# Kernel optimization log

Measured on AMD Instinct MI355X. Metric: run time of the kernel, lower is better.

The kernel has to match this reference:

```python
import jax, jax.numpy as jnp
import numpy as np

B, T_SRC, T_TGT = 2048, 32, 32
D = 512            # d_model
D_SRC, D_TGT = 100, 80
L = 2              # n_layers


def setup_inputs() -> dict:
    key = jax.random.key(0)
    ks = jax.random.split(key, 16)
    s = 1.0 / float(np.sqrt(D))  # torch LSTM init scale
    u = lambda k, shape: jax.random.uniform(k, shape, jnp.float32, -s, s)
    return {
        "src": jax.random.randint(ks[0], (B, T_SRC), 0, D_SRC, dtype=jnp.int32),
        "tgt": jax.random.randint(ks[1], (B, T_TGT), 0, D_TGT, dtype=jnp.int32),
        "enc_emb": jax.random.normal(ks[2], (D_SRC, D), jnp.float32),
        "dec_emb": jax.random.normal(ks[3], (D_TGT, D), jnp.float32),
        "enc_Wih": u(ks[4], (L, 4 * D, D)),
        "enc_Whh": u(ks[5], (L, 4 * D, D)),
        "enc_bih": u(ks[6], (L, 4 * D)),
        "enc_bhh": u(ks[7], (L, 4 * D)),
        "dec_Wih": u(ks[8], (L, 4 * D, D)),
        "dec_Whh": u(ks[9], (L, 4 * D, D)),
        "dec_bih": u(ks[10], (L, 4 * D)),
        "dec_bhh": u(ks[11], (L, 4 * D)),
        "post_W": u(ks[12], (D_TGT, D)),
        "post_b": u(ks[13], (D_TGT,)),
    }


def lstm_cell(x, h, c, Wih, Whh, bih, bhh):
    # PyTorch gate order: i, f, g, o
    gates = x @ Wih.T + bih + h @ Whh.T + bhh  # [B, 4D]
    i, f, g, o = jnp.split(gates, 4, axis=-1)
    c_new = jax.nn.sigmoid(f) * c + jax.nn.sigmoid(i) * jnp.tanh(g)
    h_new = jax.nn.sigmoid(o) * jnp.tanh(c_new)
    return h_new, c_new


def reference(src, tgt, enc_emb, dec_emb, enc_Wih, enc_Whh, enc_bih, enc_bhh,
              dec_Wih, dec_Whh, dec_bih, dec_bhh, post_W, post_b):
    # Eval-mode forward: dropout = identity, teacher forcing disabled
    # (tf = random() < ratio AND self.training is False at inference).
    n_layers = enc_Wih.shape[0]
    Bb = src.shape[0]
    Dm = enc_emb.shape[1]

    # ---- encoder: multi-layer LSTM over src embeddings ----
    x = enc_emb[src].swapaxes(0, 1)  # [T_src, B, D]
    hs, cs = [], []
    z = jnp.zeros((Bb, Dm), x.dtype)
    for l in range(n_layers):
        def step(carry, xt, l=l):
            h, c = carry
            h, c = lstm_cell(xt, h, c, enc_Wih[l], enc_Whh[l], enc_bih[l], enc_bhh[l])
            return (h, c), h
        (hT, cT), x = jax.lax.scan(step, (z, z), x)
        hs.append(hT)
        cs.append(cT)
    h0 = jnp.stack(hs)  # [L, B, D]
    c0 = jnp.stack(cs)  # [L, B, D]

    prev0 = dec_emb[tgt[:, 0]]  # [B, D]

    def dec_step(carry, _):
        h, c, prev = carry
        x = prev
        new_h, new_c = [], []
        for l in range(n_layers):
            hl, cl = lstm_cell(x, h[l], c[l], dec_Wih[l], dec_Whh[l], dec_bih[l], dec_bhh[l])
            new_h.append(hl)
            new_c.append(cl)
            x = hl
        logits = x @ post_W.T + post_b          # [B, d_tgt]
        pred = jnp.argmax(logits, axis=-1)       # [B]
        prev = dec_emb[pred]                     # [B, D]
        return (jnp.stack(new_h), jnp.stack(new_c), prev), logits

    _, out = jax.lax.scan(dec_step, (h0, c0, prev0), None, length=tgt.shape[1])
    return out.swapaxes(0, 1)  # [B, T_tgt, d_tgt]
```

## Files before the change

### kernel.cpp

```cpp
#include <hip/hip_runtime.h>
#include <hip/hip_bf16.h>

#define B_  2048
#define T_  32
#define D_  512
#define G_  2048
#define VT_ 80
#define BD  (B_ * D_)
#define LWE ((size_t)G_ * D_)

typedef _Float16 half8 __attribute__((ext_vector_type(8)));
typedef _Float16 half4_t __attribute__((ext_vector_type(4)));
typedef float    f32x4 __attribute__((ext_vector_type(4)));

static __device__ __forceinline__ float sigm(float x) {
    return 1.0f / (1.0f + expf(-x));
}

typedef __attribute__((address_space(1))) unsigned int gas_u32;
typedef __attribute__((address_space(3))) unsigned int las_u32;
static __device__ __forceinline__ void glds16(const void* src, void* dst) {
    __builtin_amdgcn_global_load_lds(
        (gas_u32*)(unsigned long long)(size_t)src,
        (las_u32*)(unsigned int)(size_t)dst, 16, 0, 0);
}

#define WB() do {                                         \
    asm volatile("s_waitcnt vmcnt(2)" ::: "memory");      \
    __builtin_amdgcn_s_barrier();                         \
    __builtin_amdgcn_sched_barrier(0);                    \
} while (0)

__global__ void zero_ws(int4* __restrict__ p, int n) {
    int i = blockIdx.x * blockDim.x + threadIdx.x;
    if (i < n) p[i] = int4{0, 0, 0, 0};
}
__global__ void init_pred(const int* __restrict__ tgt, int* __restrict__ pred) {
    int i = blockIdx.x * blockDim.x + threadIdx.x;
    if (i < B_) pred[i] = tgt[i * T_];
}

__global__ void split_weights(const float* __restrict__ s0, const float* __restrict__ s1,
                              const float* __restrict__ s2, const float* __restrict__ s3,
                              const float* __restrict__ s4, const float* __restrict__ s5,
                              _Float16* __restrict__ Wbase) {
    int g = blockIdx.x * blockDim.x + threadIdx.x;
    int mat = g >> 17;
    int rem = g & 131071;
    int np  = rem >> 6;
    int kq  = rem & 63;
    const float* src = (mat == 0) ? s0 : (mat == 1) ? s1 : (mat == 2) ? s2
                     : (mat == 3) ? s3 : (mat == 4) ? s4 : s5;
    int n = (np & 3) * D_ + (np >> 2);
    const float* sp = src + (size_t)n * D_ + kq * 8;
    float4 v0 = ((const float4*)sp)[0], v1 = ((const float4*)sp)[1];
    float x[8] = {v0.x, v0.y, v0.z, v0.w, v1.x, v1.y, v1.z, v1.w};
    _Float16 hi[8], lo[8];
    #pragma unroll
    for (int u = 0; u < 8; ++u) {
        hi[u] = (_Float16)x[u];
        lo[u] = (_Float16)(x[u] - (float)hi[u]);
    }
    int tile = (np >> 4) * 16 + (kq >> 2);
    int lane = (np & 15) | ((kq & 3) << 4);
    size_t e = (size_t)tile * 512 + (size_t)lane * 8;
    _Float16* Whi = Wbase + (size_t)mat * (2 * LWE);
    _Float16* Wlo = Whi + LWE;
    *(half8*)(Whi + e) = *(half8*)hi;
    *(half8*)(Wlo + e) = *(half8*)lo;
}

__global__ void split_postW(const float* __restrict__ pw,
                            _Float16* __restrict__ Ph, _Float16* __restrict__ Pl) {
    int g = blockIdx.x * blockDim.x + threadIdx.x;
    if (g >= VT_ * 64) return;
    int v = g >> 6, kq = g & 63;
    const float* sp = pw + (size_t)v * D_ + kq * 8;
    float4 v0 = ((const float4*)sp)[0], v1 = ((const float4*)sp)[1];
    float x[8] = {v0.x, v0.y, v0.z, v0.w, v1.x, v1.y, v1.z, v1.w};
    _Float16 hi[8], lo[8];
    #pragma unroll
    for (int u = 0; u < 8; ++u) {
        hi[u] = (_Float16)x[u];
        lo[u] = (_Float16)(x[u] - (float)hi[u]);
    }
    int tile = (v >> 4) * 16 + (kq >> 2);
    int lane = (v & 15) | ((kq & 3) << 4);
    size_t e = (size_t)tile * 512 + (size_t)lane * 8;
    *(half8*)(Ph + e) = *(half8*)hi;
    *(half8*)(Pl + e) = *(half8*)lo;
}

__global__ void perm_bias(const float* __restrict__ ebih, const float* __restrict__ ebhh,
                          const float* __restrict__ dbih, const float* __restrict__ dbhh,
                          float* __restrict__ biasP) {
    int i = blockIdx.x * blockDim.x + threadIdx.x;
    int cfg = i >> 11, np = i & 2047;
    int n = (np & 3) * D_ + (np >> 2);
    const float* bi = ((cfg < 2) ? ebih : dbih) + (cfg & 1) * G_;
    const float* bh = ((cfg < 2) ? ebhh : dbhh) + (cfg & 1) * G_;
    biasP[cfg * G_ + np] = bi[n] + bh[n];
}

__global__ __launch_bounds__(256) void compute_P(
    const float* __restrict__ enc_emb, const float* __restrict__ dec_emb,
    const float* __restrict__ encW0,   const float* __restrict__ decW0,
    float* __restrict__ P) {
    __shared__ float es[10][D_];
    __shared__ float part[4][64][10];
    int by = blockIdx.y;
    bool enc = (by < 10);
    int r0 = enc ? by * 10 : 100 + (by - 10) * 10;
    int s0 = enc ? by * 10 : (by - 10) * 10;
    const float* emb = enc ? enc_emb : dec_emb;
    const float* W   = enc ? encW0 : decW0;
    int tid = threadIdx.x;
    #pragma unroll
    for (int it = 0; it < 5; ++it) {
        int i4 = it * 256 + tid;
        int rr = i4 >> 7, cc = i4 & 127;
        ((float4*)es[rr])[cc] = ((const float4*)(emb + (size_t)(s0 + rr) * D_))[cc];
    }
    __syncthreads();
    int o   = tid & 63;
    int seg = tid >> 6;
    int np = blockIdx.x * 64 + o;
    int n = (np & 3) * D_ + (np >> 2);
    const float* wr = W + (size_t)n * D_ + seg * 128;
    float acc[10];
    #pragma unroll
    for (int rr = 0; rr < 10; ++rr) acc[rr] = 0.f;
    for (int k = 0; k < 128; k += 4) {
        float4 w4 = *(const float4*)(wr + k);
        int kb = seg * 128 + k;
        #pragma unroll
        for (int rr = 0; rr < 10; ++rr)
            acc[rr] += es[rr][kb] * w4.x + es[rr][kb+1] * w4.y
                     + es[rr][kb+2] * w4.z + es[rr][kb+3] * w4.w;
    }
    #pragma unroll
    for (int rr = 0; rr < 10; ++rr) part[seg][o][rr] = acc[rr];
    __syncthreads();
    for (int i = tid; i < 640; i += 256) {
        int o2 = i & 63, rr = i >> 6;
        P[(size_t)(r0 + rr) * G_ + blockIdx.x * 64 + o2] =
            (part[0][o2][rr] + part[1][o2][rr]) + (part[2][o2][rr] + part[3][o2][rr]);
    }
}

struct CellJob {
    const _Float16 *a0h, *a0l, *w0h, *w0l;
    int kclo0, kchi0;
    const _Float16 *a1h, *a1l, *w1h, *w1l;
    int kclo1, kchi1;
    const float *biasP;
    const float *P;
    const int  *idx;
    int idx_stride, emb_rows;
    float *c_io;
    _Float16 *hh_out, *hl_out;
};

__global__ __launch_bounds__(512, 2) void lstm_cell_mfma(CellJob J0, CellJob J1) {
    const CellJob J = (blockIdx.z == 0) ? J0 : J1;
    __shared__ __align__(128) char smem[65536];
    float (*gf)[68] = (float (*)[68])smem;

    const int tid  = threadIdx.x;
    const int w    = tid >> 6;
    const int lane = tid & 63;
    const int g    = w >> 2;
    const int mw   = w & 3;
    const int id   = blockIdx.x;
    const int bx   = id >> 3;
    const int m0   = (id & 7) * 256;

    const _Float16* Ah = g ? J.a1h : J.a0h;
    const _Float16* Al = g ? J.a1l : J.a0l;
    const _Float16* Wh = g ? J.w1h : J.w0h;
    const _Float16* Wl = g ? J.w1l : J.w0l;
    const int kclo = g ? J.kclo1 : J.kclo0;
    const int kchi = g ? J.kchi1 : J.kchi0;

    const int afr = (m0 >> 4) + mw * 4;
    const int wfr = bx * 4;

    f32x4 acc[4][4];
    #pragma unroll
    for (int i = 0; i < 4; ++i)
        #pragma unroll
        for (int j = 0; j < 4; ++j) acc[i][j] = f32x4{0.f, 0.f, 0.f, 0.f};

    char* const sb = smem + w * 2048;
    const char* const rg0 = smem + (g << 13);

    auto stage = [&](int buf, int kc) {
        size_t toff = (((size_t)(wfr + (w & 3)) * 16 + kc) << 9) + (size_t)lane * 8;
        char* d = sb + buf * 16384;
        glds16(Wh + toff, d);
        glds16(Wl + toff, d + 1024);
    };
    auto ldA = [&](half8* A8, int kc) {
        size_t lo8 = (size_t)lane * 8;
        #pragma unroll
        for (int i = 0; i < 4; ++i) {
            size_t off = (((size_t)(afr + i) * 16 + kc) << 9) + lo8;
            A8[i]     = *(const half8*)(Ah + off);
            A8[4 + i] = *(const half8*)(Al + off);
        }
    };
    auto domfma = [&](const half8* A8, int buf) {
        const char* r = rg0 + buf * 16384;
        size_t lo16 = (size_t)lane * 16;
        #pragma unroll
        for (int j = 0; j < 4; ++j) {
            half8 Bh = *(const half8*)(r + j * 2048 + lo16);
            half8 Bl = *(const half8*)(r + j * 2048 + 1024 + lo16);
            #pragma unroll
            for (int i = 0; i < 4; ++i) {
                acc[i][j] = __builtin_amdgcn_mfma_f32_16x16x32_f16(A8[i], Bh, acc[i][j], 0, 0, 0);
                acc[i][j] = __builtin_amdgcn_mfma_f32_16x16x32_f16(A8[i], Bl, acc[i][j], 0, 0, 0);
                acc[i][j] = __builtin_amdgcn_mfma_f32_16x16x32_f16(A8[4 + i], Bh, acc[i][j], 0, 0, 0);
            }
        }
    };

    half8 A0[8], A1[8];
    const int nit = (kchi - kclo) >> 2;

    ldA(A0, kclo);
    __builtin_amdgcn_sched_barrier(0);
    stage(0, kclo);
    stage(1, kclo + 1);
    WB();

    for (int it = 0; it < nit; ++it) {
        const int k0 = kclo + (it << 2);
        const bool more = (it + 1 < nit);

        ldA(A1, k0 + 1); __builtin_amdgcn_sched_barrier(0);
        stage(2, k0 + 2);
        domfma(A0, 0);
        WB();

        ldA(A0, k0 + 2); __builtin_amdgcn_sched_barrier(0);
        stage(3, k0 + 3);
        domfma(A1, 1);
        WB();

        ldA(A1, k0 + 3); __builtin_amdgcn_sched_barrier(0);
        if (more) stage(0, k0 + 4);
        domfma(A0, 2);
        WB();

        if (more) {
            ldA(A0, k0 + 4); __builtin_amdgcn_sched_barrier(0);
            stage(1, k0 + 5);
        }
        domfma(A1, 3);
        WB();
    }

    const int rbase = (lane >> 4) << 2;
    const int cbase = lane & 15;
    for (int p = 0; p < 2; ++p) {
        if (g == 0 && (mw >> 1) == p) {
            #pragma unroll
            for (int i = 0; i < 4; ++i) {
                int mrow = (mw & 1) * 64 + i * 16 + rbase;
                #pragma unroll
                for (int j = 0; j < 4; ++j) {
                    int nc = j * 16 + cbase;
                    #pragma unroll
                    for (int r = 0; r < 4; ++r)
                        gf[mrow + r][nc] = acc[i][j][r];
                }
            }
        }
        __syncthreads();
        if (g == 1 && (mw >> 1) == p) {
            #pragma unroll
            for (int i = 0; i < 4; ++i) {
                int mrow = (mw & 1) * 64 + i * 16 + rbase;
                #pragma unroll
                for (int j = 0; j < 4; ++j) {
                    int nc = j * 16 + cbase;
                    #pragma unroll
                    for (int r = 0; r < 4; ++r)
                        gf[mrow + r][nc] += acc[i][j][r];
                }
            }
        }
        __syncthreads();
        {
            int mr = tid >> 2, q = tid & 3;
            int mg = m0 + p * 128 + mr;
            const float4* brow = (const float4*)(J.biasP + (bx << 6));
            const float4* Pr = nullptr;
            if (J.P) {
                int s = J.idx[mg * J.idx_stride];
                s = min(max(s, 0), J.emb_rows - 1);
                Pr = (const float4*)(J.P + (size_t)s * G_ + (bx << 6));
            }
            float* crow = J.c_io + (size_t)mg * D_ + (bx << 4) + (q << 2);
            float4 cv = *(float4*)crow;
            _Float16 hh4[4], hl4[4];
            #pragma unroll
            for (int e = 0; e < 4; ++e) {
                int dl = (q << 2) + e;
                float4 g4 = *(float4*)&gf[mr][dl << 2];
                float4 b4 = brow[dl];
                float gi = g4.x + b4.x, gF = g4.y + b4.y;
                float gg = g4.z + b4.z, go = g4.w + b4.w;
                if (Pr) {
                    float4 p4 = Pr[dl];
                    gi += p4.x; gF += p4.y; gg += p4.z; go += p4.w;
                }
                float cc = (&cv.x)[e];
                float cn = sigm(gF) * cc + sigm(gi) * tanhf(gg);
                float hn = sigm(go) * tanhf(cn);
                (&cv.x)[e] = cn;
                _Float16 hH = (_Float16)hn;
                hh4[e] = hH;
                hl4[e] = (_Float16)(hn - (float)hH);
            }
            *(float4*)crow = cv;
            int kk = (bx << 4) + (q << 2);
            size_t hoff = ((size_t)((mg >> 4) * 16 + (kk >> 5)) << 9)
                        + (size_t)((mg & 15) | (((kk >> 3) & 3) << 4)) * 8
                        + ((q & 1) << 2);
            *(half4_t*)(J.hh_out + hoff) = *(half4_t*)hh4;
            *(half4_t*)(J.hl_out + hoff) = *(half4_t*)hl4;
        }
        __syncthreads();
    }
}

__global__ __launch_bounds__(128) void logits_mfma(
    const _Float16* __restrict__ Ah, const _Float16* __restrict__ Al,
    const _Float16* __restrict__ Bh, const _Float16* __restrict__ Bl,
    const float* __restrict__ postb, float* __restrict__ out,
    int t, int* __restrict__ pred) {
    __shared__ float gf2[64][85];
    __shared__ float pb[VT_];
    const int tid = threadIdx.x;
    const int w = tid >> 6;
    const int lane = tid & 63;
    const int m0 = blockIdx.x * 64;
    const int afr = blockIdx.x * 4;

    f32x4 acc[4][5];
    #pragma unroll
    for (int i = 0; i < 4; ++i)
        #pragma unroll
        for (int j = 0; j < 5; ++j) acc[i][j] = f32x4{0.f, 0.f, 0.f, 0.f};

    size_t lo8 = (size_t)lane * 8;
    for (int kc = w * 8; kc < w * 8 + 8; ++kc) {
        half8 A8[8], Bh8[5], Bl8[5];
        #pragma unroll
        for (int i = 0; i < 4; ++i) {
            size_t off = (((size_t)(afr + i) * 16 + kc) << 9) + lo8;
            A8[i]     = *(const half8*)(Ah + off);
            A8[4 + i] = *(const half8*)(Al + off);
        }
        #pragma unroll
        for (int j = 0; j < 5; ++j) {
            size_t off = (((size_t)(j * 16 + kc)) << 9) + lo8;
            Bh8[j] = *(const half8*)(Bh + off);
            Bl8[j] = *(const half8*)(Bl + off);
        }
        #pragma unroll
        for (int i = 0; i < 4; ++i)
            #pragma unroll
            for (int j = 0; j < 5; ++j) {
                acc[i][j] = __builtin_amdgcn_mfma_f32_16x16x32_f16(A8[i], Bh8[j], acc[i][j], 0, 0, 0);
                acc[i][j] = __builtin_amdgcn_mfma_f32_16x16x32_f16(A8[i], Bl8[j], acc[i][j], 0, 0, 0);
                acc[i][j] = __builtin_amdgcn_mfma_f32_16x16x32_f16(A8[4 + i], Bh8[j], acc[i][j], 0, 0, 0);
            }
    }

    if (tid < VT_) pb[tid] = postb[tid];
    const int quad = lane >> 4, c = lane & 15;
    if (w == 0) {
        #pragma unroll
        for (int i = 0; i < 4; ++i)
            #pragma unroll
            for (int j = 0; j < 5; ++j)
                #pragma unroll
                for (int r = 0; r < 4; ++r)
                    gf2[i * 16 + quad * 4 + r][j * 16 + c] = acc[i][j][r];
    }
    __syncthreads();
    if (w == 1) {
        #pragma unroll
        for (int i = 0; i < 4; ++i)
            #pragma unroll
            for (int j = 0; j < 5; ++j)
                #pragma unroll
                for (int r = 0; r < 4; ++r)
                    gf2[i * 16 + quad * 4 + r][j * 16 + c] += acc[i][j][r];
    }
    __syncthreads();
    if (tid < 64) {
        int r = tid;
        float best = -3.4e38f; int bi = 0;
        #pragma unroll
        for (int v = 0; v < VT_; ++v) {
            float x = gf2[r][v] + pb[v];
            if (x > best) { best = x; bi = v; }
        }
        pred[m0 + r] = bi;
        float* orow = out + (size_t)(m0 + r) * (T_ * VT_) + (size_t)t * VT_;
        #pragma unroll
        for (int v4 = 0; v4 < VT_ / 4; ++v4) {
            float4 g4 = *(float4*)&gf2[r][v4 * 4];
            float4 b4 = *(float4*)&pb[v4 * 4];
            float4 o4 = {g4.x + b4.x, g4.y + b4.y, g4.z + b4.z, g4.w + b4.w};
            *(float4*)(orow + v4 * 4) = o4;
        }
    }
}

extern "C" void kernel_launch(void* const* d_in, const int* in_sizes, int n_in,
                              void* d_out, int out_size, void* d_ws, size_t ws_size,
                              hipStream_t stream) {
    (void)in_sizes; (void)n_in; (void)out_size; (void)ws_size;

    const int*   src     = (const int*)d_in[0];
    const int*   tgt     = (const int*)d_in[1];
    const float* enc_emb = (const float*)d_in[2];
    const float* dec_emb = (const float*)d_in[3];
    const float* enc_Wih = (const float*)d_in[4];
    const float* enc_Whh = (const float*)d_in[5];
    const float* enc_bih = (const float*)d_in[6];
    const float* enc_bhh = (const float*)d_in[7];
    const float* dec_Wih = (const float*)d_in[8];
    const float* dec_Whh = (const float*)d_in[9];
    const float* dec_bih = (const float*)d_in[10];
    const float* dec_bhh = (const float*)d_in[11];
    const float* post_W  = (const float*)d_in[12];
    const float* post_b  = (const float*)d_in[13];

    char* wsb = (char*)d_ws;
    int*   pred  = (int*)wsb;
    float* biasB = (float*)(wsb + 16384);
    float* Ptab  = (float*)(wsb + 16384 + 32768);
    char*  zbase = wsb + 16384 + 32768 + 180 * G_ * 4;
    float* C0 = (float*)zbase;
    float* C1 = C0 + BD;
    _Float16* Hh00 = (_Float16*)(C1 + BD);
    _Float16* Hh10 = Hh00 + BD;
    _Float16* Hl00 = Hh10 + BD;
    _Float16* Hl10 = Hl00 + BD;
    _Float16* Hh01 = Hl10 + BD;
    _Float16* Hh11 = Hh01 + BD;
    _Float16* Hl01 = Hh11 + BD;
    _Float16* Hl11 = Hl01 + BD;
    _Float16* Wb   = Hl11 + BD;
    _Float16* PwH  = Wb + 6 * 2 * LWE;
    _Float16* PwL  = PwH + (size_t)VT_ * D_;

    _Float16* Hhi[2][2] = { { Hh00, Hh01 }, { Hh10, Hh11 } };
    _Float16* Hlo[2][2] = { { Hl00, Hl01 }, { Hl10, Hl11 } };
    float*    Cp[2]     = { C0, C1 };
    auto WP = [&](int m, int pl) { return Wb + (size_t)m * (2 * LWE) + (size_t)pl * LWE; };

    float* out = (float*)d_out;

    zero_ws<<<4096, 256, 0, stream>>>((int4*)zbase, (16 * 1024 * 1024) / 16);
    init_pred<<<8, 256, 0, stream>>>(tgt, pred);
    split_weights<<<3072, 256, 0, stream>>>(
        enc_Whh, enc_Wih + LWE, enc_Whh + LWE,
        dec_Whh, dec_Wih + LWE, dec_Whh + LWE, Wb);
    split_postW<<<20, 256, 0, stream>>>(post_W, PwH, PwL);
    perm_bias<<<32, 256, 0, stream>>>(enc_bih, enc_bhh, dec_bih, dec_bhh, biasB);
    {
        dim3 gP(32, 18);
        compute_P<<<gP, 256, 0, stream>>>(enc_emb, dec_emb, enc_Wih, dec_Wih, Ptab);
    }

    dim3 grid1(256, 1, 1);
    dim3 grid2(256, 1, 2);
    int c0 = 0, c1 = 0;

    auto mkL0 = [&](bool enc, const int* ix, int stride, int rows) {
        int m = enc ? 0 : 3;
        CellJob j;
        j.a0h = Hhi[0][c0]; j.a0l = Hlo[0][c0];
        j.w0h = WP(m, 0);   j.w0l = WP(m, 1);
        j.kclo0 = 0; j.kchi0 = 8;
        j.a1h = Hhi[0][c0]; j.a1l = Hlo[0][c0];
        j.w1h = WP(m, 0);   j.w1l = WP(m, 1);
        j.kclo1 = 8; j.kchi1 = 16;
        j.biasP = biasB + (enc ? 0 : 2) * G_;
        j.P = enc ? Ptab : Ptab + (size_t)100 * G_;
        j.idx = ix; j.idx_stride = stride; j.emb_rows = rows;
        j.c_io = Cp[0];
        j.hh_out = Hhi[0][c0 ^ 1]; j.hl_out = Hlo[0][c0 ^ 1];
        return j;
    };
    auto mkL1 = [&](bool enc) {
        int mi = enc ? 1 : 4, mh = enc ? 2 : 5;
        CellJob j;
        j.a0h = Hhi[0][c0]; j.a0l = Hlo[0][c0];
        j.w0h = WP(mi, 0);  j.w0l = WP(mi, 1);
        j.kclo0 = 0; j.kchi0 = 16;
        j.a1h = Hhi[1][c1]; j.a1l = Hlo[1][c1];
        j.w1h = WP(mh, 0);  j.w1l = WP(mh, 1);
        j.kclo1 = 0; j.kchi1 = 16;
        j.biasP = biasB + (enc ? 1 : 3) * G_;
        j.P = nullptr; j.idx = nullptr; j.idx_stride = 0; j.emb_rows = 0;
        j.c_io = Cp[1];
        j.hh_out = Hhi[1][c1 ^ 1]; j.hl_out = Hlo[1][c1 ^ 1];
        return j;
    };

    {
        CellJob j0 = mkL0(true, src + 0, T_, 100);
        lstm_cell_mfma<<<grid1, 512, 0, stream>>>(j0, j0);
        c0 ^= 1;
        for (int t = 0; t < T_ - 1; ++t) {
            CellJob jA = mkL1(true);
            CellJob jB = mkL0(true, src + t + 1, T_, 100);
            lstm_cell_mfma<<<grid2, 512, 0, stream>>>(jA, jB);
            c1 ^= 1; c0 ^= 1;
        }
        CellJob jZ = mkL1(true);
        lstm_cell_mfma<<<grid1, 512, 0, stream>>>(jZ, jZ);
        c1 ^= 1;
    }

    for (int t = 0; t < T_; ++t) {
        CellJob j0 = mkL0(false, pred, 1, VT_);
        lstm_cell_mfma<<<grid1, 512, 0, stream>>>(j0, j0);
        c0 ^= 1;
        CellJob j1 = mkL1(false);
        lstm_cell_mfma<<<grid1, 512, 0, stream>>>(j1, j1);
        c1 ^= 1;
        logits_mfma<<<32, 128, 0, stream>>>(
            Hhi[1][c1], Hlo[1][c1], PwH, PwL, post_b, out, t, pred);
    }
}
```

Measured before the change: 4.273 ms.

## Deepen LSTM load pipeline, remap blocks per XCD, and split logits across more blocks

The LSTM cell kernel's wait drops from vmcnt(2) to vmcnt(10), so more global loads stay in flight across barriers. It also removes the interior sched_barriers and the last-iteration guards, and drains all loads after the loop. Block IDs are remapped so that blocks on the same XCD share batch/column tiles, aiming for better L2 reuse. The logits kernel goes from 32 blocks of 128 threads to 128 single-wave blocks of 16 rows each, which removes the cross-wave reduction and raises parallelism. Without the guards, the last iteration issues loads past kchi, which risks out-of-range reads, and vmcnt(10) relies on the exact number of outstanding loads being right.

```diff
diff --git a/kernel.cpp b/kernel.cpp
--- a/kernel.cpp
+++ b/kernel.cpp
@@ -25,8 +25,8 @@
         (las_u32*)(unsigned int)(size_t)dst, 16, 0, 0);
 }
 
-#define WB() do {                                         \
-    asm volatile("s_waitcnt vmcnt(2)" ::: "memory");      \
+#define WBX() do {                                        \
+    asm volatile("s_waitcnt vmcnt(10)" ::: "memory");     \
     __builtin_amdgcn_s_barrier();                         \
     __builtin_amdgcn_sched_barrier(0);                    \
 } while (0)
@@ -172,8 +172,11 @@
     const int g    = w >> 2;
     const int mw   = w & 3;
     const int id   = blockIdx.x;
-    const int bx   = id >> 3;
-    const int m0   = (id & 7) * 256;
+    const int xcd  = id & 7;
+    const int rest = id >> 3;
+    const int mt   = ((rest & 3) << 1) | (xcd >> 2);
+    const int bx   = ((rest >> 2) << 2) | (xcd & 3);
+    const int m0   = mt * 256;
 
     const _Float16* Ah = g ? J.a1h : J.a0h;
     const _Float16* Al = g ? J.a1l : J.a0l;
@@ -229,37 +232,21 @@
     const int nit = (kchi - kclo) >> 2;
 
     ldA(A0, kclo);
-    __builtin_amdgcn_sched_barrier(0);
     stage(0, kclo);
     stage(1, kclo + 1);
-    WB();
+    asm volatile("s_waitcnt vmcnt(0)" ::: "memory");
+    __builtin_amdgcn_s_barrier();
+    __builtin_amdgcn_sched_barrier(0);
 
     for (int it = 0; it < nit; ++it) {
         const int k0 = kclo + (it << 2);
-        const bool more = (it + 1 < nit);
-
-        ldA(A1, k0 + 1); __builtin_amdgcn_sched_barrier(0);
-        stage(2, k0 + 2);
-        domfma(A0, 0);
-        WB();
-
-        ldA(A0, k0 + 2); __builtin_amdgcn_sched_barrier(0);
-        stage(3, k0 + 3);
-        domfma(A1, 1);
-        WB();
-
-        ldA(A1, k0 + 3); __builtin_amdgcn_sched_barrier(0);
-        if (more) stage(0, k0 + 4);
-        domfma(A0, 2);
-        WB();
-
-        if (more) {
-            ldA(A0, k0 + 4); __builtin_amdgcn_sched_barrier(0);
-            stage(1, k0 + 5);
-        }
-        domfma(A1, 3);
-        WB();
-    }
+        ldA(A1, k0 + 1); stage(2, k0 + 2); domfma(A0, 0); WBX();
+        ldA(A0, k0 + 2); stage(3, k0 + 3); domfma(A1, 1); WBX();
+        ldA(A1, k0 + 3); stage(0, k0 + 4); domfma(A0, 2); WBX();
+        ldA(A0, k0 + 4); stage(1, k0 + 5); domfma(A1, 3); WBX();
+    }
+    asm volatile("s_waitcnt vmcnt(0)" ::: "memory");
+    __syncthreads();
 
     const int rbase = (lane >> 4) << 2;
     const int cbase = lane & 15;
@@ -336,33 +323,28 @@
     }
 }
 
-__global__ __launch_bounds__(128) void logits_mfma(
+__global__ __launch_bounds__(64) void logits_mfma(
     const _Float16* __restrict__ Ah, const _Float16* __restrict__ Al,
     const _Float16* __restrict__ Bh, const _Float16* __restrict__ Bl,
     const float* __restrict__ postb, float* __restrict__ out,
     int t, int* __restrict__ pred) {
-    __shared__ float gf2[64][85];
+    __shared__ float gf2[16][85];
     __shared__ float pb[VT_];
-    const int tid = threadIdx.x;
-    const int w = tid >> 6;
-    const int lane = tid & 63;
-    const int m0 = blockIdx.x * 64;
-    const int afr = blockIdx.x * 4;
-
-    f32x4 acc[4][5];
-    #pragma unroll
-    for (int i = 0; i < 4; ++i)
-        #pragma unroll
-        for (int j = 0; j < 5; ++j) acc[i][j] = f32x4{0.f, 0.f, 0.f, 0.f};
+    const int lane = threadIdx.x;
+    const int m0  = blockIdx.x * 16;
+    const int afr = blockIdx.x;
+
+    f32x4 acc[5];
+    #pragma unroll
+    for (int j = 0; j < 5; ++j) acc[j] = f32x4{0.f, 0.f, 0.f, 0.f};
 
     size_t lo8 = (size_t)lane * 8;
-    for (int kc = w * 8; kc < w * 8 + 8; ++kc) {
-        half8 A8[8], Bh8[5], Bl8[5];
-        #pragma unroll
-        for (int i = 0; i < 4; ++i) {
-            size_t off = (((size_t)(afr + i) * 16 + kc) << 9) + lo8;
-            A8[i]     = *(const half8*)(Ah + off);
-            A8[4 + i] = *(const half8*)(Al + off);
+    for (int kc = 0; kc < 16; ++kc) {
+        half8 Ahh, All, Bh8[5], Bl8[5];
+        {
+            size_t off = (((size_t)afr * 16 + kc) << 9) + lo8;
+            Ahh = *(const half8*)(Ah + off);
+            All = *(const half8*)(Al + off);
         }
         #pragma unroll
         for (int j = 0; j < 5; ++j) {
@@ -371,39 +353,23 @@
             Bl8[j] = *(const half8*)(Bl + off);
         }
         #pragma unroll
-        for (int i = 0; i < 4; ++i)
-            #pragma unroll
-            for (int j = 0; j < 5; ++j) {
-                acc[i][j] = __builtin_amdgcn_mfma_f32_16x16x32_f16(A8[i], Bh8[j], acc[i][j], 0, 0, 0);
-                acc[i][j] = __builtin_amdgcn_mfma_f32_16x16x32_f16(A8[i], Bl8[j], acc[i][j], 0, 0, 0);
-                acc[i][j] = __builtin_amdgcn_mfma_f32_16x16x32_f16(A8[4 + i], Bh8[j], acc[i][j], 0, 0, 0);
-            }
-    }
-
-    if (tid < VT_) pb[tid] = postb[tid];
+        for (int j = 0; j < 5; ++j) {
+            acc[j] = __builtin_amdgcn_mfma_f32_16x16x32_f16(Ahh, Bh8[j], acc[j], 0, 0, 0);
+            acc[j] = __builtin_amdgcn_mfma_f32_16x16x32_f16(Ahh, Bl8[j], acc[j], 0, 0, 0);
+            acc[j] = __builtin_amdgcn_mfma_f32_16x16x32_f16(All, Bh8[j], acc[j], 0, 0, 0);
+        }
+    }
+
+    if (lane < 40) ((float2*)pb)[lane] = ((const float2*)postb)[lane];
     const int quad = lane >> 4, c = lane & 15;
-    if (w == 0) {
-        #pragma unroll
-        for (int i = 0; i < 4; ++i)
-            #pragma unroll
-            for (int j = 0; j < 5; ++j)
-                #pragma unroll
-                for (int r = 0; r < 4; ++r)
-                    gf2[i * 16 + quad * 4 + r][j * 16 + c] = acc[i][j][r];
-    }
+    #pragma unroll
+    for (int j = 0; j < 5; ++j)
+        #pragma unroll
+        for (int r = 0; r < 4; ++r)
+            gf2[quad * 4 + r][j * 16 + c] = acc[j][r];
     __syncthreads();
-    if (w == 1) {
-        #pragma unroll
-        for (int i = 0; i < 4; ++i)
-            #pragma unroll
-            for (int j = 0; j < 5; ++j)
-                #pragma unroll
-                for (int r = 0; r < 4; ++r)
-                    gf2[i * 16 + quad * 4 + r][j * 16 + c] += acc[i][j][r];
-    }
-    __syncthreads();
-    if (tid < 64) {
-        int r = tid;
+    if (lane < 16) {
+        int r = lane;
         float best = -3.4e38f; int bi = 0;
         #pragma unroll
         for (int v = 0; v < VT_; ++v) {
@@ -538,7 +504,7 @@
         CellJob j1 = mkL1(false);
         lstm_cell_mfma<<<grid1, 512, 0, stream>>>(j1, j1);
         c1 ^= 1;
-        logits_mfma<<<32, 128, 0, stream>>>(
+        logits_mfma<<<128, 64, 0, stream>>>(
             Hhi[1][c1], Hlo[1][c1], PwH, PwL, post_b, out, t, pred);
     }
 }
```

After: 4.603 ms. 7.7% more time.
